# Kernel optimization log

Measured on AMD Instinct MI355X. Metric: run time of the kernel, lower is better.

The kernel has to match this reference:

```python
import jax, jax.numpy as jnp
import numpy as np

D_MODEL = 768
D_FF = 3072
N_HEADS = 12
D_QUART = D_MODEL // 4  # 192
EPS = 1e-5


def layer_norm(x, g, b):
    mu = jnp.mean(x, axis=-1, keepdims=True)
    var = jnp.mean((x - mu) ** 2, axis=-1, keepdims=True)
    return (x - mu) * jax.lax.rsqrt(var + EPS) * g + b


def setup_inputs() -> dict:
    key = jax.random.key(0)
    ks = jax.random.split(key, 24)
    d, dff, dq = D_MODEL, D_FF, D_QUART
    s = lambda k, shape, fan: jax.random.normal(k, shape, jnp.float32) * (1.0 / np.sqrt(fan))
    return {
        "x": jax.random.normal(ks[0], (8, 1024, d), jnp.float32),
        # distance_proj: Linear(1, d//4) -> weight [dq], bias [dq]
        "dp_w": s(ks[1], (dq,), 1), "dp_b": jnp.zeros((dq,), jnp.float32),
        # spatial_encoding: Linear(d,d) GELU Linear(d,d)
        "se_w1": s(ks[2], (d, d), d), "se_b1": jnp.zeros((d,), jnp.float32),
        "se_w2": s(ks[3], (d, d), d), "se_b2": jnp.zeros((d,), jnp.float32),
        # attention projections (stored [in, out])
        "wq": s(ks[4], (d, d), d), "bq": jnp.zeros((d,), jnp.float32),
        "wk": s(ks[5], (d, d), d), "bk": jnp.zeros((d,), jnp.float32),
        "wv": s(ks[6], (d, d), d), "bv": jnp.zeros((d,), jnp.float32),
        "wo": s(ks[7], (d, d), d), "bo": jnp.zeros((d,), jnp.float32),
        # geometric_net FFN
        "gw1": s(ks[8], (d, dff), d), "gb1": jnp.zeros((dff,), jnp.float32),
        "gw2": s(ks[9], (dff, d), dff), "gb2": jnp.zeros((d,), jnp.float32),
        # layer norms
        "n1_g": jnp.ones((d,), jnp.float32), "n1_b": jnp.zeros((d,), jnp.float32),
        "n2_g": jnp.ones((d,), jnp.float32), "n2_b": jnp.zeros((d,), jnp.float32),
    }


def _forward(x, dp_w, dp_b, se_w1, se_b1, se_w2, se_b2,
             wq, bq, wk, bk, wv, bv, wo, bo,
             gw1, gb1, gw2, gb2, n1_g, n1_b, n2_g, n2_b):
    B, N, d = x.shape
    # --- compute_spatial_features ---
    # ||x_i - x_j|| via Gram trick (avoids [B,N,N,d] intermediate)
    sq = jnp.sum(x * x, axis=-1)                      # [B,N]
    gram = jnp.einsum('bnd,bmd->bnm', x, x)           # [B,N,N]
    d2 = jnp.maximum(sq[:, :, None] + sq[:, None, :] - 2.0 * gram, 0.0)
    dist = jnp.sqrt(d2)                               # [B,N,N]
    # Linear(1, d/4) then mean over j commutes: project the mean distance
    mean_d = jnp.mean(dist, axis=2)                   # [B,N]
    spat = mean_d[..., None] * dp_w + dp_b            # [B,N,d/4]
    spat = jnp.pad(spat, ((0, 0), (0, 0), (0, d - D_QUART)))  # [B,N,d]
    # spatial_encoding MLP (exact GELU, matching torch nn.GELU default)
    h = jax.nn.gelu(spat @ se_w1 + se_b1, approximate=False)
    x = x + (h @ se_w2 + se_b2)
    # --- attention block ---
    res = x
    xn = layer_norm(x, n1_g, n1_b)
    H, dh = N_HEADS, d // N_HEADS
    q = (xn @ wq + bq).reshape(B, N, H, dh)
    k = (xn @ wk + bk).reshape(B, N, H, dh)
    v = (xn @ wv + bv).reshape(B, N, H, dh)
    scores = jnp.einsum('bqhd,bkhd->bhqk', q, k) / np.sqrt(dh)
    attn = jax.nn.softmax(scores, axis=-1)
    o = jnp.einsum('bhqk,bkhd->bqhd', attn, v).reshape(B, N, d)
    x = res + (o @ wo + bo)
    # --- FFN block ---
    res = x
    xn = layer_norm(x, n2_g, n2_b)
    h = jax.nn.gelu(xn @ gw1 + gb1, approximate=False)
    x = res + (h @ gw2 + gb2)
    return x


def reference(x, dp_w, dp_b, se_w1, se_b1, se_w2, se_b2,
              wq, bq, wk, bk, wv, bv, wo, bo,
              gw1, gb1, gw2, gb2, n1_g, n1_b, n2_g, n2_b):
    return _forward(x, dp_w, dp_b, se_w1, se_b1, se_w2, se_b2,
                    wq, bq, wk, bk, wv, bv, wo, bo,
                    gw1, gb1, gw2, gb2, n1_g, n1_b, n2_g, n2_b)
```

## Files before the change

### kernel.cpp

```cpp
#include <hip/hip_runtime.h>
#include <hip/hip_bf16.h>

typedef unsigned short ushort;
typedef __attribute__((ext_vector_type(8))) __bf16 bf16x8;
typedef __attribute__((ext_vector_type(4))) float f32x4;
typedef __attribute__((ext_vector_type(8))) ushort ushort8;

__device__ inline ushort f2bf(float f) {
    union { float f; unsigned u; } a{f};
    unsigned r = a.u + 0x7FFFu + ((a.u >> 16) & 1u);
    return (ushort)(r >> 16);
}
__device__ inline float gelu_f(float x) {
    return 0.5f * x * (1.f + erff(x * 0.70710678118654752f));
}

__global__ void transpose_to_bf16(const float* __restrict__ Wm, ushort* __restrict__ Wt, int K, int N) {
    __shared__ float tile[32][33];
    int k0 = blockIdx.x * 32, n0 = blockIdx.y * 32;
    int tx = threadIdx.x, ty = threadIdx.y;
    #pragma unroll
    for (int r = ty; r < 32; r += 8) tile[r][tx] = Wm[(size_t)(k0 + r) * N + n0 + tx];
    __syncthreads();
    #pragma unroll
    for (int r = ty; r < 32; r += 8) Wt[(size_t)(n0 + r) * K + k0 + tx] = f2bf(tile[tx][r]);
}

__global__ void rowstat(const float* __restrict__ x, ushort* __restrict__ xb, float* __restrict__ sq) {
    int row = blockIdx.x;
    const float* xr = x + (size_t)row * 768;
    ushort* xbr = xb + (size_t)row * 768;
    int t = threadIdx.x;
    float s = 0.f;
    #pragma unroll
    for (int i = 0; i < 3; ++i) {
        float vv = xr[t + i * 256];
        xbr[t + i * 256] = f2bf(vv);
        s += vv * vv;
    }
    #pragma unroll
    for (int off = 1; off < 64; off <<= 1) s += __shfl_xor(s, off);
    __shared__ float wsum[4];
    if ((t & 63) == 0) wsum[t >> 6] = s;
    __syncthreads();
    if (t == 0) sq[row] = wsum[0] + wsum[1] + wsum[2] + wsum[3];
}

__global__ void precomp_ac(const float* __restrict__ dp_w, const float* __restrict__ dp_b,
                           const float* __restrict__ se_w1, const float* __restrict__ se_b1,
                           float* __restrict__ Avec, float* __restrict__ Cvec) {
    int o = blockIdx.x * 256 + threadIdx.x;
    float a = 0.f, c = 0.f;
    for (int i = 0; i < 192; ++i) {
        float w = se_w1[(size_t)i * 768 + o];
        a += dp_w[i] * w;
        c += dp_b[i] * w;
    }
    Avec[o] = a;
    Cvec[o] = c + se_b1[o];
}

__global__ void hgen(const float* __restrict__ mean_acc, const float* __restrict__ Avec,
                     const float* __restrict__ Cvec, ushort* __restrict__ h) {
    int row = blockIdx.x;
    float md = mean_acc[row] * (1.f / 1024.f);
    int t = threadIdx.x;
    #pragma unroll
    for (int i = 0; i < 3; ++i) {
        int o = t + i * 256;
        h[(size_t)row * 768 + o] = f2bf(gelu_f(md * Avec[o] + Cvec[o]));
    }
}

__global__ void lnorm(const float* __restrict__ xin, const float* __restrict__ g,
                      const float* __restrict__ b, ushort* __restrict__ xn) {
    int row = blockIdx.x;
    const float* xr = xin + (size_t)row * 768;
    int t = threadIdx.x;
    float v[3];
    float s = 0.f, s2 = 0.f;
    #pragma unroll
    for (int i = 0; i < 3; ++i) {
        v[i] = xr[t + i * 256];
        s += v[i];
        s2 += v[i] * v[i];
    }
    #pragma unroll
    for (int off = 1; off < 64; off <<= 1) { s += __shfl_xor(s, off); s2 += __shfl_xor(s2, off); }
    __shared__ float a0[4], a1[4];
    if ((t & 63) == 0) { a0[t >> 6] = s; a1[t >> 6] = s2; }
    __syncthreads();
    s = a0[0] + a0[1] + a0[2] + a0[3];
    s2 = a1[0] + a1[1] + a1[2] + a1[3];
    float mu = s * (1.f / 768.f);
    float var = s2 * (1.f / 768.f) - mu * mu;
    float rs = rsqrtf(var + 1e-5f);
    #pragma unroll
    for (int i = 0; i < 3; ++i) {
        int o = t + i * 256;
        xn[(size_t)row * 768 + o] = f2bf((v[i] - mu) * rs * g[o] + b[o]);
    }
}

#define BM 128
#define BK 32

enum { EPI_BF16 = 0, EPI_GELU = 1, EPI_RES = 2, EPI_GRAM = 3, EPI_QKV = 4 };

template <int EPI, int BNT>
__launch_bounds__(256, BNT == 64 ? 4 : 2)
__global__ void gemm_bt(const ushort* __restrict__ A, const ushort* __restrict__ Bt,
                        int M, int N, int K,
                        const float* __restrict__ bias,
                        const float* res, float* outf,
                        ushort* __restrict__ outh,
                        const float* __restrict__ sq, float* __restrict__ mean_acc) {
    __shared__ __align__(16) ushort As[2][BM * BK];
    __shared__ __align__(16) ushort Bs[2][BNT * BK];

    unsigned gx = gridDim.x, gy = gridDim.y;
    unsigned flat = blockIdx.x + gx * (blockIdx.y + gy * blockIdx.z);
    unsigned total = gx * gy * gridDim.z;
    unsigned chunk = total >> 3;
    flat = (flat & 7) * chunk + (flat >> 3);
    unsigned bx = flat % gx;
    unsigned rem = flat / gx;
    unsigned by = rem % gy;
    unsigned bz = rem / gy;

    int m0 = bx * BM;
    int n0 = by * BNT;
    if (EPI == EPI_GRAM) {
        A += (size_t)bz * 1024 * 768;
        Bt = A;
        sq += bz * 1024;
        mean_acc += bz * 1024;
    }
    int t = threadIdx.x, w = t >> 6, l = t & 63;
    int lg = l >> 4, li = l & 15;
    constexpr int MI = (BNT == 128) ? 4 : 2;
    int wm = (BNT == 128) ? (w >> 1) * 64 : w * 32;
    int wn = (BNT == 128) ? (w & 1) * 64 : 0;

    int srow = l >> 2, scol = (l & 3) * 8;
    const ushort* agp0 = A + (size_t)(m0 + (2 * w) * 16 + srow) * K + scol;
    const ushort* agp1 = A + (size_t)(m0 + (2 * w + 1) * 16 + srow) * K + scol;
    const ushort* bgp0;
    const ushort* bgp1 = nullptr;
    ushort* la0 = &As[0][(2 * w) * 16 * BK];
    ushort* lb0;
    if (BNT == 128) {
        bgp0 = Bt + (size_t)(n0 + (2 * w) * 16 + srow) * K + scol;
        bgp1 = Bt + (size_t)(n0 + (2 * w + 1) * 16 + srow) * K + scol;
        lb0 = &Bs[0][(2 * w) * 16 * BK];
    } else {
        bgp0 = Bt + (size_t)(n0 + w * 16 + srow) * K + scol;
        lb0 = &Bs[0][w * 16 * BK];
    }

    f32x4 acc[MI][4] = {};

    auto stage = [&](int buf, int kt) {
        size_t ko = (size_t)kt * BK;
        ushort* la = la0 + buf * (BM * BK);
        ushort* lb = lb0 + buf * (BNT * BK);
        __builtin_amdgcn_global_load_lds((const __attribute__((address_space(1))) void*)(agp0 + ko),
                                         (__attribute__((address_space(3))) void*)la, 16, 0, 0);
        __builtin_amdgcn_global_load_lds((const __attribute__((address_space(1))) void*)(agp1 + ko),
                                         (__attribute__((address_space(3))) void*)(la + 16 * BK), 16, 0, 0);
        __builtin_amdgcn_global_load_lds((const __attribute__((address_space(1))) void*)(bgp0 + ko),
                                         (__attribute__((address_space(3))) void*)lb, 16, 0, 0);
        if (BNT == 128)
            __builtin_amdgcn_global_load_lds((const __attribute__((address_space(1))) void*)(bgp1 + ko),
                                             (__attribute__((address_space(3))) void*)(lb + 16 * BK), 16, 0, 0);
    };

    int nk = K / BK;
    stage(0, 0);
    __syncthreads();
    int buf = 0;
    for (int kt = 0; kt < nk; ++kt) {
        if (kt + 1 < nk) stage(buf ^ 1, kt + 1);
        bf16x8 af[MI], bfr[4];
        #pragma unroll
        for (int i = 0; i < MI; ++i)
            af[i] = *reinterpret_cast<const bf16x8*>(&As[buf][(wm + i * 16 + li) * BK + lg * 8]);
        #pragma unroll
        for (int i = 0; i < 4; ++i)
            bfr[i] = *reinterpret_cast<const bf16x8*>(&Bs[buf][(wn + i * 16 + li) * BK + lg * 8]);
        #pragma unroll
        for (int mi = 0; mi < MI; ++mi)
            #pragma unroll
            for (int ni = 0; ni < 4; ++ni)
                acc[mi][ni] = __builtin_amdgcn_mfma_f32_16x16x32_bf16(af[mi], bfr[ni], acc[mi][ni], 0, 0, 0);
        __syncthreads();
        buf ^= 1;
    }

    #pragma unroll
    for (int mi = 0; mi < MI; ++mi) {
        #pragma unroll
        for (int r = 0; r < 4; ++r) {
            int row = m0 + wm + mi * 16 + lg * 4 + r;
            if (EPI == EPI_GRAM) {
                float si = sq[row];
                float s = 0.f;
                #pragma unroll
                for (int ni = 0; ni < 4; ++ni) {
                    int col = n0 + wn + ni * 16 + li;
                    float d2 = si + sq[col] - 2.f * acc[mi][ni][r];
                    s += sqrtf(fmaxf(d2, 0.f));
                }
                s += __shfl_xor(s, 1); s += __shfl_xor(s, 2);
                s += __shfl_xor(s, 4); s += __shfl_xor(s, 8);
                if (li == 0) atomicAdd(&mean_acc[row], s);
            } else {
                #pragma unroll
                for (int ni = 0; ni < 4; ++ni) {
                    int col = n0 + wn + ni * 16 + li;
                    float v = acc[mi][ni][r] + bias[col];
                    if (EPI == EPI_BF16) outh[(size_t)row * N + col] = f2bf(v);
                    if (EPI == EPI_GELU) outh[(size_t)row * N + col] = f2bf(gelu_f(v));
                    if (EPI == EPI_RES) outf[(size_t)row * N + col] = res[(size_t)row * N + col] + v;
                    if (EPI == EPI_QKV) {
                        int which = col / 768;
                        int c2 = col - which * 768;
                        outh[(size_t)which * (8192 * 768) + (size_t)row * 768 + c2] = f2bf(v);
                    }
                }
            }
        }
    }
}

template <int EPI>
__launch_bounds__(512, 2)
__global__ void gemm8(const ushort* __restrict__ A, const ushort* __restrict__ Bt,
                      int M, int N, int K,
                      const float* __restrict__ bias,
                      const float* res, float* outf, ushort* __restrict__ outh) {
    __shared__ __align__(16) ushort As[3][2][128 * 64];
    __shared__ __align__(16) ushort Bs[3][2][64 * 64];

    unsigned gx = gridDim.x;
    unsigned orig = blockIdx.x + gx * blockIdx.y;
    unsigned xcd = orig & 7;
    unsigned q = orig >> 3;
    unsigned mpg = gx >> 3;
    unsigned mloc = q % mpg;
    unsigned n = q / mpg;
    int m0 = (xcd * mpg + mloc) * 256;
    int n0 = n * 128;

    int t = threadIdx.x, w = t >> 6, l = t & 63;
    int lg = l >> 4, li = l & 15;
    int wr = w >> 1, wc = w & 1;
    int ha = wr >> 1;
    int ra = (wr & 1) * 64;

    f32x4 acc[4][4] = {};

    auto stage = [&](int buf, int kt) {
        int k0 = kt * 64;
        #pragma unroll
        for (int h = 0; h < 2; ++h) {
            #pragma unroll
            for (int jj = 0; jj < 2; ++jj) {
                int d = (2 * w + jj) * 1024 + l * 16;
                int dp = d ^ (((d >> 7) & 7) << 4);
                const ushort* src = A + (size_t)(m0 + h * 128 + (dp >> 7)) * K + k0 + ((dp & 127) >> 1);
                __builtin_amdgcn_global_load_lds(
                    (const __attribute__((address_space(1))) void*)src,
                    (__attribute__((address_space(3))) void*)&As[buf][h][(2 * w + jj) * 512], 16, 0, 0);
            }
            {
                int d = w * 1024 + l * 16;
                int dp = d ^ (((d >> 7) & 7) << 4);
                const ushort* src = Bt + (size_t)(n0 + h * 64 + (dp >> 7)) * K + k0 + ((dp & 127) >> 1);
                __builtin_amdgcn_global_load_lds(
                    (const __attribute__((address_space(1))) void*)src,
                    (__attribute__((address_space(3))) void*)&Bs[buf][h][w * 512], 16, 0, 0);
            }
        }
    };

    int nk = K / 64;
    stage(0, 0);
    stage(1, 1);
    stage(2, 2);
    for (int kt = 0; kt < nk; ++kt) {
        int buf = kt % 3;
        if (kt + 2 < nk)      asm volatile("s_waitcnt vmcnt(12)" ::: "memory");
        else if (kt + 1 < nk) asm volatile("s_waitcnt vmcnt(6)" ::: "memory");
        else                  asm volatile("s_waitcnt vmcnt(0)" ::: "memory");
        asm volatile("s_barrier" ::: "memory");
        __builtin_amdgcn_sched_barrier(0);
        #pragma unroll
        for (int kk = 0; kk < 2; ++kk) {
            bf16x8 af[4], bf[4];
            #pragma unroll
            for (int mi = 0; mi < 4; ++mi) {
                int e = (ra + mi * 16 + li) * 128 + kk * 64 + lg * 16;
                int ep = e ^ (((e >> 7) & 7) << 4);
                af[mi] = *reinterpret_cast<const bf16x8*>(&As[buf][ha][ep >> 1]);
            }
            #pragma unroll
            for (int ni = 0; ni < 4; ++ni) {
                int e = (ni * 16 + li) * 128 + kk * 64 + lg * 16;
                int ep = e ^ (((e >> 7) & 7) << 4);
                bf[ni] = *reinterpret_cast<const bf16x8*>(&Bs[buf][wc][ep >> 1]);
            }
            __builtin_amdgcn_s_setprio(1);
            #pragma unroll
            for (int mi = 0; mi < 4; ++mi)
                #pragma unroll
                for (int ni = 0; ni < 4; ++ni)
                    acc[mi][ni] = __builtin_amdgcn_mfma_f32_16x16x32_bf16(af[mi], bf[ni], acc[mi][ni], 0, 0, 0);
            __builtin_amdgcn_s_setprio(0);
        }
        asm volatile("s_barrier" ::: "memory");
        __builtin_amdgcn_sched_barrier(0);
        if (kt + 3 < nk) stage(buf, kt + 3);
    }

    #pragma unroll
    for (int mi = 0; mi < 4; ++mi) {
        #pragma unroll
        for (int r = 0; r < 4; ++r) {
            int row = m0 + wr * 64 + mi * 16 + lg * 4 + r;
            #pragma unroll
            for (int ni = 0; ni < 4; ++ni) {
                int col = n0 + wc * 64 + ni * 16 + li;
                float v = acc[mi][ni][r] + bias[col];
                if (EPI == EPI_GELU) outh[(size_t)row * N + col] = f2bf(gelu_f(v));
                if (EPI == EPI_RES)  outf[(size_t)row * N + col] = res[(size_t)row * N + col] + v;
                if (EPI == EPI_QKV) {
                    int which = col / 768;
                    int c2 = col - which * 768;
                    outh[(size_t)which * (8192 * 768) + (size_t)row * 768 + c2] = f2bf(v);
                }
            }
        }
    }
}

__launch_bounds__(256, 3)
__global__ void flash_attn(const ushort* __restrict__ q, const ushort* __restrict__ k,
                           const ushort* __restrict__ v, ushort* __restrict__ o) {
    int flat = blockIdx.x + 8 * (blockIdx.y + 12 * blockIdx.z);
    flat = (flat & 7) * 96 + (flat >> 3);
    int qt = flat & 7;
    int rem = flat >> 3;
    int h = rem % 12;
    int b = rem / 12;

    int t = threadIdx.x, w = t >> 6, l = t & 63;
    int lg = l >> 4, li = l & 15;

    __shared__ __align__(16) ushort Vt[2][64][72];
    __shared__ __align__(16) ushort P[4][32][72];

    const size_t hoff = (size_t)h * 64;
    const size_t bbase = (size_t)b * 1024 * 768;

    bf16x8 qf[2][2];
    #pragma unroll
    for (int f = 0; f < 2; ++f) {
        int qrow = qt * 128 + w * 32 + f * 16 + li;
        const ushort* qp = &q[bbase + (size_t)qrow * 768 + hoff];
        qf[f][0] = *reinterpret_cast<const bf16x8*>(qp + lg * 8);
        qf[f][1] = *reinterpret_cast<const bf16x8*>(qp + 32 + lg * 8);
    }

    bf16x8 onesf;
    #pragma unroll
    for (int i = 0; i < 8; ++i) onesf[i] = (__bf16)1.0f;

    float m_[2][4];
    f32x4 oacc[2][4];
    f32x4 oell[2];
    #pragma unroll
    for (int f = 0; f < 2; ++f) {
        #pragma unroll
        for (int r = 0; r < 4; ++r) m_[f][r] = -1e30f;
        oell[f] = f32x4{0.f, 0.f, 0.f, 0.f};
        #pragma unroll
        for (int n = 0; n < 4; ++n) oacc[f][n] = f32x4{0.f, 0.f, 0.f, 0.f};
    }

    int vrow = t & 63;
    int vc = t >> 6;
    const ushort* vbase = &v[bbase + hoff];

    ushort8 vv0 = *reinterpret_cast<const ushort8*>(&vbase[(size_t)vrow * 768 + vc * 8]);
    ushort8 vv1 = *reinterpret_cast<const ushort8*>(&vbase[(size_t)vrow * 768 + (vc + 4) * 8]);

    for (int jt = 0; jt < 16; ++jt) {
        int j0 = jt * 64, buf = jt & 1;
        #pragma unroll
        for (int i = 0; i < 8; ++i) Vt[buf][vc * 8 + i][vrow] = vv0[i];
        #pragma unroll
        for (int i = 0; i < 8; ++i) Vt[buf][(vc + 4) * 8 + i][vrow] = vv1[i];
        if (jt < 15) {
            vv0 = *reinterpret_cast<const ushort8*>(&vbase[(size_t)(j0 + 64 + vrow) * 768 + vc * 8]);
            vv1 = *reinterpret_cast<const ushort8*>(&vbase[(size_t)(j0 + 64 + vrow) * 768 + (vc + 4) * 8]);
        }
        bf16x8 kf0[4], kf1[4];
        #pragma unroll
        for (int jj = 0; jj < 4; ++jj) {
            const ushort* kp = &k[bbase + (size_t)(j0 + jj * 16 + li) * 768 + hoff];
            kf0[jj] = *reinterpret_cast<const bf16x8*>(kp + lg * 8);
            kf1[jj] = *reinterpret_cast<const bf16x8*>(kp + 32 + lg * 8);
        }
        f32x4 s[2][4];
        #pragma unroll
        for (int jj = 0; jj < 4; ++jj)
            #pragma unroll
            for (int f = 0; f < 2; ++f) {
                f32x4 a = {0.f, 0.f, 0.f, 0.f};
                a = __builtin_amdgcn_mfma_f32_16x16x32_bf16(qf[f][0], kf0[jj], a, 0, 0, 0);
                a = __builtin_amdgcn_mfma_f32_16x16x32_bf16(qf[f][1], kf1[jj], a, 0, 0, 0);
                s[f][jj] = a * 0.125f;
            }
        #pragma unroll
        for (int f = 0; f < 2; ++f) {
            float mt[4];
            #pragma unroll
            for (int r = 0; r < 4; ++r)
                mt[r] = fmaxf(fmaxf(s[f][0][r], s[f][1][r]), fmaxf(s[f][2][r], s[f][3][r]));
            #pragma unroll
            for (int r = 0; r < 4; ++r) {
                mt[r] = fmaxf(mt[r], __shfl_xor(mt[r], 1));
                mt[r] = fmaxf(mt[r], __shfl_xor(mt[r], 2));
                mt[r] = fmaxf(mt[r], __shfl_xor(mt[r], 4));
                mt[r] = fmaxf(mt[r], __shfl_xor(mt[r], 8));
            }
            bool need = (mt[0] > m_[f][0] + 8.f) | (mt[1] > m_[f][1] + 8.f) |
                        (mt[2] > m_[f][2] + 8.f) | (mt[3] > m_[f][3] + 8.f);
            if (__any(need)) {
                #pragma unroll
                for (int r = 0; r < 4; ++r) {
                    float mn = fmaxf(m_[f][r], mt[r]);
                    float al = __expf(m_[f][r] - mn);
                    m_[f][r] = mn;
                    #pragma unroll
                    for (int n = 0; n < 4; ++n) oacc[f][n][r] *= al;
                    oell[f][r] *= al;
                }
            }
            #pragma unroll
            for (int jj = 0; jj < 4; ++jj)
                #pragma unroll
                for (int r = 0; r < 4; ++r)
                    P[w][f * 16 + lg * 4 + r][jj * 16 + li] = f2bf(__expf(s[f][jj][r] - m_[f][r]));
        }
        __syncthreads();
        bf16x8 pf[2][2];
        #pragma unroll
        for (int f = 0; f < 2; ++f) {
            pf[f][0] = *reinterpret_cast<const bf16x8*>(&P[w][f * 16 + li][lg * 8]);
            pf[f][1] = *reinterpret_cast<const bf16x8*>(&P[w][f * 16 + li][32 + lg * 8]);
        }
        #pragma unroll
        for (int f = 0; f < 2; ++f) {
            oell[f] = __builtin_amdgcn_mfma_f32_16x16x32_bf16(pf[f][0], onesf, oell[f], 0, 0, 0);
            oell[f] = __builtin_amdgcn_mfma_f32_16x16x32_bf16(pf[f][1], onesf, oell[f], 0, 0, 0);
        }
        #pragma unroll
        for (int n = 0; n < 4; ++n) {
            bf16x8 vf0 = *reinterpret_cast<const bf16x8*>(&Vt[buf][n * 16 + li][lg * 8]);
            bf16x8 vf1 = *reinterpret_cast<const bf16x8*>(&Vt[buf][n * 16 + li][32 + lg * 8]);
            #pragma unroll
            for (int f = 0; f < 2; ++f) {
                oacc[f][n] = __builtin_amdgcn_mfma_f32_16x16x32_bf16(pf[f][0], vf0, oacc[f][n], 0, 0, 0);
                oacc[f][n] = __builtin_amdgcn_mfma_f32_16x16x32_bf16(pf[f][1], vf1, oacc[f][n], 0, 0, 0);
            }
        }
    }
    #pragma unroll
    for (int f = 0; f < 2; ++f)
        #pragma unroll
        for (int n = 0; n < 4; ++n)
            #pragma unroll
            for (int r = 0; r < 4; ++r) {
                int row = qt * 128 + w * 32 + f * 16 + lg * 4 + r;
                o[bbase + (size_t)row * 768 + hoff + n * 16 + li] = f2bf(oacc[f][n][r] / oell[f][r]);
            }
}

extern "C" void kernel_launch(void* const* d_in, const int* in_sizes, int n_in,
                              void* d_out, int out_size, void* d_ws, size_t ws_size,
                              hipStream_t stream) {
    const float* x = (const float*)d_in[0];
    const float* dp_w = (const float*)d_in[1];
    const float* dp_b = (const float*)d_in[2];
    const float* se_w1 = (const float*)d_in[3];
    const float* se_b1 = (const float*)d_in[4];
    const float* se_w2 = (const float*)d_in[5];
    const float* se_b2 = (const float*)d_in[6];
    const float* wq = (const float*)d_in[7];  const float* bq = (const float*)d_in[8];
    const float* wk = (const float*)d_in[9];  const float* bk = (const float*)d_in[10];
    const float* wv = (const float*)d_in[11]; const float* bv = (const float*)d_in[12];
    const float* wo = (const float*)d_in[13]; const float* bo = (const float*)d_in[14];
    const float* gw1 = (const float*)d_in[15]; const float* gb1 = (const float*)d_in[16];
    const float* gw2 = (const float*)d_in[17]; const float* gb2 = (const float*)d_in[18];
    const float* n1g = (const float*)d_in[19]; const float* n1b = (const float*)d_in[20];
    const float* n2g = (const float*)d_in[21]; const float* n2b = (const float*)d_in[22];
    float* out = (float*)d_out;

    constexpr size_t SZ_ACT = (size_t)8192 * 768 * 2;
    char* W = (char*)d_ws;
    ushort* xb = (ushort*)(W);
    ushort* q_ = (ushort*)(W + SZ_ACT);
    ushort* k_ = (ushort*)(W + 2 * SZ_ACT);
    ushort* v_ = (ushort*)(W + 3 * SZ_ACT);
    ushort* o_ = (ushort*)(W + 4 * SZ_ACT);
    ushort* hsp = q_;
    ushort* hff = q_;
    ushort* wqt = (ushort*)(W + 5 * SZ_ACT);
    ushort* wkt = wqt + (size_t)768 * 768;
    ushort* wvt = wkt + (size_t)768 * 768;
    ushort* wot = wvt + (size_t)768 * 768;
    ushort* sw2t = wot + (size_t)768 * 768;
    ushort* g1t = sw2t + (size_t)768 * 768;
    ushort* g2t = g1t + (size_t)768 * 3072;
    float* sqv = (float*)(g2t + (size_t)3072 * 768);
    float* meanv = sqv + 8192;
    float* Avec = meanv + 8192;
    float* Cvec = Avec + 768;
    float* bqkv = Cvec + 768;

    dim3 tb(32, 8);
    transpose_to_bf16<<<dim3(24, 24), tb, 0, stream>>>(se_w2, sw2t, 768, 768);
    transpose_to_bf16<<<dim3(24, 24), tb, 0, stream>>>(wq, wqt, 768, 768);
    transpose_to_bf16<<<dim3(24, 24), tb, 0, stream>>>(wk, wkt, 768, 768);
    transpose_to_bf16<<<dim3(24, 24), tb, 0, stream>>>(wv, wvt, 768, 768);
    transpose_to_bf16<<<dim3(24, 24), tb, 0, stream>>>(wo, wot, 768, 768);
    transpose_to_bf16<<<dim3(24, 96), tb, 0, stream>>>(gw1, g1t, 768, 3072);
    transpose_to_bf16<<<dim3(96, 24), tb, 0, stream>>>(gw2, g2t, 3072, 768);
    hipMemcpyAsync(bqkv, bq, 768 * sizeof(float), hipMemcpyDeviceToDevice, stream);
    hipMemcpyAsync(bqkv + 768, bk, 768 * sizeof(float), hipMemcpyDeviceToDevice, stream);
    hipMemcpyAsync(bqkv + 1536, bv, 768 * sizeof(float), hipMemcpyDeviceToDevice, stream);

    rowstat<<<8192, 256, 0, stream>>>(x, xb, sqv);
    precomp_ac<<<3, 256, 0, stream>>>(dp_w, dp_b, se_w1, se_b1, Avec, Cvec);
    hipMemsetAsync(meanv, 0, 8192 * sizeof(float), stream);

    gemm_bt<EPI_GRAM, 128><<<dim3(8, 8, 8), 256, 0, stream>>>(xb, xb, 1024, 1024, 768,
                                                              nullptr, nullptr, nullptr, nullptr, sqv, meanv);
    hgen<<<8192, 256, 0, stream>>>(meanv, Avec, Cvec, hsp);
    gemm8<EPI_RES><<<dim3(32, 6), 512, 0, stream>>>(hsp, sw2t, 8192, 768, 768,
                                                    se_b2, x, out, nullptr);
    lnorm<<<8192, 256, 0, stream>>>(out, n1g, n1b, xb);
    gemm8<EPI_QKV><<<dim3(32, 18), 512, 0, stream>>>(xb, wqt, 8192, 2304, 768,
                                                     bqkv, nullptr, nullptr, q_);
    flash_attn<<<dim3(8, 12, 8), 256, 0, stream>>>(q_, k_, v_, o_);
    gemm8<EPI_RES><<<dim3(32, 6), 512, 0, stream>>>(o_, wot, 8192, 768, 768,
                                                    bo, out, out, nullptr);
    lnorm<<<8192, 256, 0, stream>>>(out, n2g, n2b, xb);
    gemm8<EPI_GELU><<<dim3(32, 24), 512, 0, stream>>>(xb, g1t, 8192, 3072, 768,
                                                      gb1, nullptr, nullptr, hff);
    gemm8<EPI_RES><<<dim3(32, 6), 512, 0, stream>>>(hff, g2t, 8192, 768, 3072,
                                                    gb2, out, out, nullptr);
}
```

Measured before the change: 458.9 us.

## Halve gemm8 K-tile to 32 and raise occupancy to four blocks per CU

Cuts the gemm8 K-step from 64 to 32, which halves the LDS footprint of the triple-buffered A/B stages. It also raises launch bounds from 2 to 4 blocks per CU and replaces the XOR swizzle with one suited to 64-byte rows. The wait counts are adjusted to match. The aim is more resident waves to hide memory latency, at the cost of twice as many barrier-synchronised iterations, fewer MFMAs between barriers, and a tighter register budget that may cause spills.

```diff
diff --git a/kernel.cpp b/kernel.cpp
--- a/kernel.cpp
+++ b/kernel.cpp
@@ -234,13 +234,13 @@
 }
 
 template <int EPI>
-__launch_bounds__(512, 2)
+__launch_bounds__(512, 4)
 __global__ void gemm8(const ushort* __restrict__ A, const ushort* __restrict__ Bt,
                       int M, int N, int K,
                       const float* __restrict__ bias,
                       const float* res, float* outf, ushort* __restrict__ outh) {
-    __shared__ __align__(16) ushort As[3][2][128 * 64];
-    __shared__ __align__(16) ushort Bs[3][2][64 * 64];
+    __shared__ __align__(16) ushort As[3][2][128 * 32];
+    __shared__ __align__(16) ushort Bs[3][128 * 32];
 
     unsigned gx = gridDim.x;
     unsigned orig = blockIdx.x + gx * blockIdx.y;
@@ -261,63 +261,56 @@
     f32x4 acc[4][4] = {};
 
     auto stage = [&](int buf, int kt) {
-        int k0 = kt * 64;
+        int k0 = kt * 32;
+        int d = w * 1024 + l * 16;
+        int dp = d ^ ((((d >> 6) ^ (d >> 8)) & 3) << 4);
+        int srow = dp >> 6, scol = (dp & 63) >> 1;
         #pragma unroll
         for (int h = 0; h < 2; ++h) {
-            #pragma unroll
-            for (int jj = 0; jj < 2; ++jj) {
-                int d = (2 * w + jj) * 1024 + l * 16;
-                int dp = d ^ (((d >> 7) & 7) << 4);
-                const ushort* src = A + (size_t)(m0 + h * 128 + (dp >> 7)) * K + k0 + ((dp & 127) >> 1);
-                __builtin_amdgcn_global_load_lds(
-                    (const __attribute__((address_space(1))) void*)src,
-                    (__attribute__((address_space(3))) void*)&As[buf][h][(2 * w + jj) * 512], 16, 0, 0);
-            }
-            {
-                int d = w * 1024 + l * 16;
-                int dp = d ^ (((d >> 7) & 7) << 4);
-                const ushort* src = Bt + (size_t)(n0 + h * 64 + (dp >> 7)) * K + k0 + ((dp & 127) >> 1);
-                __builtin_amdgcn_global_load_lds(
-                    (const __attribute__((address_space(1))) void*)src,
-                    (__attribute__((address_space(3))) void*)&Bs[buf][h][w * 512], 16, 0, 0);
-            }
+            const ushort* src = A + (size_t)(m0 + h * 128 + srow) * K + k0 + scol;
+            __builtin_amdgcn_global_load_lds(
+                (const __attribute__((address_space(1))) void*)src,
+                (__attribute__((address_space(3))) void*)&As[buf][h][w * 512], 16, 0, 0);
+        }
+        {
+            const ushort* src = Bt + (size_t)(n0 + srow) * K + k0 + scol;
+            __builtin_amdgcn_global_load_lds(
+                (const __attribute__((address_space(1))) void*)src,
+                (__attribute__((address_space(3))) void*)&Bs[buf][w * 512], 16, 0, 0);
         }
     };
 
-    int nk = K / 64;
+    int nk = K / 32;
     stage(0, 0);
     stage(1, 1);
     stage(2, 2);
     for (int kt = 0; kt < nk; ++kt) {
         int buf = kt % 3;
-        if (kt + 2 < nk)      asm volatile("s_waitcnt vmcnt(12)" ::: "memory");
-        else if (kt + 1 < nk) asm volatile("s_waitcnt vmcnt(6)" ::: "memory");
+        if (kt + 2 < nk)      asm volatile("s_waitcnt vmcnt(6)" ::: "memory");
+        else if (kt + 1 < nk) asm volatile("s_waitcnt vmcnt(3)" ::: "memory");
         else                  asm volatile("s_waitcnt vmcnt(0)" ::: "memory");
         asm volatile("s_barrier" ::: "memory");
         __builtin_amdgcn_sched_barrier(0);
-        #pragma unroll
-        for (int kk = 0; kk < 2; ++kk) {
-            bf16x8 af[4], bf[4];
-            #pragma unroll
-            for (int mi = 0; mi < 4; ++mi) {
-                int e = (ra + mi * 16 + li) * 128 + kk * 64 + lg * 16;
-                int ep = e ^ (((e >> 7) & 7) << 4);
-                af[mi] = *reinterpret_cast<const bf16x8*>(&As[buf][ha][ep >> 1]);
-            }
-            #pragma unroll
-            for (int ni = 0; ni < 4; ++ni) {
-                int e = (ni * 16 + li) * 128 + kk * 64 + lg * 16;
-                int ep = e ^ (((e >> 7) & 7) << 4);
-                bf[ni] = *reinterpret_cast<const bf16x8*>(&Bs[buf][wc][ep >> 1]);
-            }
-            __builtin_amdgcn_s_setprio(1);
-            #pragma unroll
-            for (int mi = 0; mi < 4; ++mi)
-                #pragma unroll
-                for (int ni = 0; ni < 4; ++ni)
-                    acc[mi][ni] = __builtin_amdgcn_mfma_f32_16x16x32_bf16(af[mi], bf[ni], acc[mi][ni], 0, 0, 0);
-            __builtin_amdgcn_s_setprio(0);
-        }
+        bf16x8 af[4], bf[4];
+        #pragma unroll
+        for (int mi = 0; mi < 4; ++mi) {
+            int e = (ra + mi * 16 + li) * 64 + lg * 16;
+            int ep = e ^ ((((e >> 6) ^ (e >> 8)) & 3) << 4);
+            af[mi] = *reinterpret_cast<const bf16x8*>((const char*)&As[buf][ha][0] + ep);
+        }
+        #pragma unroll
+        for (int ni = 0; ni < 4; ++ni) {
+            int e = (wc * 64 + ni * 16 + li) * 64 + lg * 16;
+            int ep = e ^ ((((e >> 6) ^ (e >> 8)) & 3) << 4);
+            bf[ni] = *reinterpret_cast<const bf16x8*>((const char*)&Bs[buf][0] + ep);
+        }
+        __builtin_amdgcn_s_setprio(1);
+        #pragma unroll
+        for (int mi = 0; mi < 4; ++mi)
+            #pragma unroll
+            for (int ni = 0; ni < 4; ++ni)
+                acc[mi][ni] = __builtin_amdgcn_mfma_f32_16x16x32_bf16(af[mi], bf[ni], acc[mi][ni], 0, 0, 0);
+        __builtin_amdgcn_s_setprio(0);
         asm volatile("s_barrier" ::: "memory");
         __builtin_amdgcn_sched_barrier(0);
         if (kt + 3 < nk) stage(buf, kt + 3);
```

Result: slower. 472.8 us (+3.0%).
